# Optimization experiments

Measured on AMD Instinct MI355X. Metric: run time of the kernel, lower is better.

The kernel has to match this reference:

```python
import jax, jax.numpy as jnp
import numpy as np

N, M, KNN, KUP, POS_DIM = 15872, 35637, 5, 20, 32


def _pos_emb_table(n, d):
    # transformer-style sinusoidal table (matches PosEmb._define_pos_emb)
    pos = np.arange(n, dtype=np.float32)[:, None]
    i2 = np.arange(0, d, 2, dtype=np.float32)
    div = 10000.0 ** (i2 / d)
    pe = np.zeros((n, d), dtype=np.float32)
    pe[:, 0::2] = np.sin(pos / div)
    pe[:, 1::2] = np.cos(pos / div)
    return jnp.asarray(pe)


def _lrelu(x):
    return jnp.where(x > 0, x, 0.2 * x)


def _gather(x, idx):
    # x: [B,n,d], idx: [B,m,k] -> [B,m,k,d]
    return jax.vmap(lambda xb, ib: xb[ib])(x, idx)


def _knn_idx(x, k):
    # x: [B,n,d]; k nearest excluding self (torch knn drops column 0 of topk)
    xx = jnp.sum(x * x, axis=-1)
    neg = 2.0 * jnp.einsum('bnd,bmd->bnm', x, x) - xx[:, :, None] - xx[:, None, :]
    _, idx = jax.lax.top_k(neg, k + 1)
    return idx[..., 1:]


def _emb_block(feat, idx, ec_w1, ec_s1, ec_h1, ec_w2, ec_b2,
               w1, s1, h1, w2, s2, h2, w3, s3, h3, w4, b4):
    # get_graph_feature: [B,n,k,2*in] = cat(nbr - ctr, ctr)
    nbr = _gather(feat, idx)
    ctr = jnp.broadcast_to(feat[:, :, None, :], nbr.shape)
    e = jnp.concatenate([nbr - ctr, ctr], axis=-1)
    # edge_conv (1x1 conv2d = per-edge linear); BN folded into scale/shift (eval mode)
    e = _lrelu(jnp.einsum('bnkc,oc->bnko', e, ec_w1) * ec_s1 + ec_h1)
    e = jnp.einsum('bnkc,oc->bnko', e, ec_w2) + ec_b2
    f1 = jnp.max(e, axis=2)                                   # max over k neighbors -> [B,n,out]
    fmax = jnp.broadcast_to(jnp.max(f1, axis=1, keepdims=True), f1.shape)
    favg = jnp.broadcast_to(jnp.mean(f1, axis=1, keepdims=True), f1.shape)
    h = jnp.concatenate([feat, f1, fmax, favg], axis=-1)      # [B,n,3*out+in]
    # fc_out: 1x1 conv1d stack = per-point MLP with folded BN + LeakyReLU
    h = _lrelu(h @ w1.T * s1 + h1)
    h = _lrelu(h @ w2.T * s2 + h2)
    h = _lrelu(h @ w3.T * s3 + h3)
    return h @ w4.T + b4


def _forward(lx, ldx, pos_emb,
             b0_ec_w1, b0_ec_s1, b0_ec_h1, b0_ec_w2, b0_ec_b2,
             b0_fc_w1, b0_fc_s1, b0_fc_h1, b0_fc_w2, b0_fc_s2, b0_fc_h2,
             b0_fc_w3, b0_fc_s3, b0_fc_h3, b0_fc_w4, b0_fc_b4,
             b1_ec_w1, b1_ec_s1, b1_ec_h1, b1_ec_w2, b1_ec_b2,
             b1_fc_w1, b1_fc_s1, b1_fc_h1, b1_fc_w2, b1_fc_s2, b1_fc_h2,
             b1_fc_w3, b1_fc_s3, b1_fc_h3, b1_fc_w4, b1_fc_b4,
             up_inputs, up_w0, up_s0, up_h0, up_w_rest, up_s_rest, up_h_rest, up_wf, up_bf,
             dec_w0, dec_b0, dec_w1, dec_b1, dec_w2, dec_b2, dec_w3, dec_b3,
             dec_w4, dec_b4, dec_wf, dec_bf,
             idx0, up_idx):
    B = ldx.shape[0]
    feat_in = jnp.concatenate([ldx, jnp.broadcast_to(pos_emb[None], (B,) + pos_emb.shape)], axis=-1)  # [B,N,35]
    f0 = _emb_block(feat_in, idx0,
                    b0_ec_w1, b0_ec_s1, b0_ec_h1, b0_ec_w2, b0_ec_b2,
                    b0_fc_w1, b0_fc_s1, b0_fc_h1, b0_fc_w2, b0_fc_s2, b0_fc_h2,
                    b0_fc_w3, b0_fc_s3, b0_fc_h3, b0_fc_w4, b0_fc_b4)   # [B,N,64]
    idx1 = _knn_idx(f0, KNN)                                            # dynamic feature-space KNN
    f1 = _emb_block(f0, idx1,
                    b1_ec_w1, b1_ec_s1, b1_ec_h1, b1_ec_w2, b1_ec_b2,
                    b1_fc_w1, b1_fc_s1, b1_fc_h1, b1_fc_w2, b1_fc_s2, b1_fc_h2,
                    b1_fc_w3, b1_fc_s3, b1_fc_h3, b1_fc_w4, b1_fc_b4)   # [B,N,128]
    x_feat = jnp.concatenate([feat_in, f0, f1], axis=-1)                # [B,N,227]
    # Upscale: SIREN-activated 1x1-conv stack -> softmax interpolation weights over KUP lo-res nbrs
    h = jnp.sin(jnp.einsum('bmkc,oc->bmko', up_inputs[:B], up_w0) * up_s0 + up_h0)
    for i in range(up_w_rest.shape[0]):
        h = jnp.sin(jnp.einsum('bmkc,oc->bmko', h, up_w_rest[i]) * up_s_rest[i] + up_h_rest[i])
    logits = jnp.einsum('bmkc,oc->bmko', h, up_wf) + up_bf              # [B,M,KUP,1]
    w = jax.nn.softmax(logits, axis=2)
    grouped = _gather(x_feat, up_idx)                                   # [B,M,KUP,227]
    z = jnp.sum(w * grouped, axis=2)                                    # [B,M,227]
    # SIREN decoder: dims [227,256,128,64,32,16,3]; zip with 5 mods applies first 5 layers + head
    h = jnp.sin(30.0 * (z @ dec_w0.T + dec_b0))
    h = jnp.sin(h @ dec_w1.T + dec_b1)
    h = jnp.sin(h @ dec_w2.T + dec_b2)
    h = jnp.sin(h @ dec_w3.T + dec_b3)
    h = jnp.sin(h @ dec_w4.T + dec_b4)
    return h @ dec_wf.T + dec_bf                                        # [B,M,3]


def setup_inputs():
    key = jax.random.key(0)
    ks = iter(jax.random.split(key, 100))
    def rn(*s):
        return jax.random.normal(next(ks), s, jnp.float32) * 0.05
    def sc(*s):
        return jax.random.uniform(next(ks), s, jnp.float32, minval=0.5, maxval=1.5)
    inp = {}
    inp['lx'] = jax.random.normal(next(ks), (1, N, 3), jnp.float32)
    inp['ldx'] = jax.random.normal(next(ks), (1, N, 3), jnp.float32)
    inp['pos_emb'] = _pos_emb_table(N, POS_DIM)
    inp['idx0'] = jax.random.randint(next(ks), (1, N, KNN), 0, N - 1)
    # EmbModule 0: in=35, out=64
    inp['b0_ec_w1'], inp['b0_ec_s1'], inp['b0_ec_h1'] = rn(128, 70), sc(128), rn(128)
    inp['b0_ec_w2'], inp['b0_ec_b2'] = rn(64, 128), rn(64)
    inp['b0_fc_w1'], inp['b0_fc_s1'], inp['b0_fc_h1'] = rn(192, 227), sc(192), rn(192)
    inp['b0_fc_w2'], inp['b0_fc_s2'], inp['b0_fc_h2'] = rn(128, 192), sc(128), rn(128)
    inp['b0_fc_w3'], inp['b0_fc_s3'], inp['b0_fc_h3'] = rn(64, 128), sc(64), rn(64)
    inp['b0_fc_w4'], inp['b0_fc_b4'] = rn(64, 64), rn(64)
    # EmbModule 1: in=64, out=128
    inp['b1_ec_w1'], inp['b1_ec_s1'], inp['b1_ec_h1'] = rn(256, 128), sc(256), rn(256)
    inp['b1_ec_w2'], inp['b1_ec_b2'] = rn(128, 256), rn(128)
    inp['b1_fc_w1'], inp['b1_fc_s1'], inp['b1_fc_h1'] = rn(384, 448), sc(384), rn(384)
    inp['b1_fc_w2'], inp['b1_fc_s2'], inp['b1_fc_h2'] = rn(256, 384), sc(256), rn(256)
    inp['b1_fc_w3'], inp['b1_fc_s3'], inp['b1_fc_h3'] = rn(128, 256), sc(128), rn(128)
    inp['b1_fc_w4'], inp['b1_fc_b4'] = rn(128, 128), rn(128)
    inp['up_inputs'] = jax.random.uniform(next(ks), (1, M, KUP, 7), jnp.float32)
    inp['up_idx'] = jax.random.randint(next(ks), (1, M, KUP), 0, N - 1)
    inp['up_w0'], inp['up_s0'], inp['up_h0'] = rn(128, 7), sc(128), rn(128)
    inp['up_w_rest'], inp['up_s_rest'], inp['up_h_rest'] = rn(7, 128, 128), sc(7, 128), rn(7, 128)
    inp['up_wf'], inp['up_bf'] = rn(1, 128), rn(1)
    # SIREN decoder
    dd = [227, 256, 128, 64, 32, 16]
    for i in range(5):
        inp['dec_w%d' % i], inp['dec_b%d' % i] = rn(dd[i + 1], dd[i]), rn(dd[i + 1])
    inp['dec_wf'], inp['dec_bf'] = rn(3, 16), rn(3)
    return inp


def reference(lx, ldx, pos_emb, idx0,
              b0_ec_w1, b0_ec_s1, b0_ec_h1, b0_ec_w2, b0_ec_b2,
              b0_fc_w1, b0_fc_s1, b0_fc_h1, b0_fc_w2, b0_fc_s2, b0_fc_h2,
              b0_fc_w3, b0_fc_s3, b0_fc_h3, b0_fc_w4, b0_fc_b4,
              b1_ec_w1, b1_ec_s1, b1_ec_h1, b1_ec_w2, b1_ec_b2,
              b1_fc_w1, b1_fc_s1, b1_fc_h1, b1_fc_w2, b1_fc_s2, b1_fc_h2,
              b1_fc_w3, b1_fc_s3, b1_fc_h3, b1_fc_w4, b1_fc_b4,
              up_inputs, up_idx, up_w0, up_s0, up_h0,
              up_w_rest, up_s_rest, up_h_rest, up_wf, up_bf,
              dec_w0, dec_b0, dec_w1, dec_b1, dec_w2, dec_b2, dec_w3, dec_b3,
              dec_w4, dec_b4, dec_wf, dec_bf):
    return _forward(lx, ldx, pos_emb,
                    b0_ec_w1, b0_ec_s1, b0_ec_h1, b0_ec_w2, b0_ec_b2,
                    b0_fc_w1, b0_fc_s1, b0_fc_h1, b0_fc_w2, b0_fc_s2, b0_fc_h2,
                    b0_fc_w3, b0_fc_s3, b0_fc_h3, b0_fc_w4, b0_fc_b4,
                    b1_ec_w1, b1_ec_s1, b1_ec_h1, b1_ec_w2, b1_ec_b2,
                    b1_fc_w1, b1_fc_s1, b1_fc_h1, b1_fc_w2, b1_fc_s2, b1_fc_h2,
                    b1_fc_w3, b1_fc_s3, b1_fc_h3, b1_fc_w4, b1_fc_b4,
                    up_inputs, up_w0, up_s0, up_h0, up_w_rest, up_s_rest, up_h_rest, up_wf, up_bf,
                    dec_w0, dec_b0, dec_w1, dec_b1, dec_w2, dec_b2, dec_w3, dec_b3,
                    dec_w4, dec_b4, dec_wf, dec_bf,
                    idx0, up_idx)
```

## Files before the change

kernel.cpp:

```cpp
#include <hip/hip_runtime.h>
#include <hip/hip_bf16.h>
#include <math.h>

#define N_PTS 15872
#define M_PTS 35637
#define KNN_K 5
#define KUP   20
#define UP_ROWS (M_PTS * KUP)
#define NTILE (N_PTS/32)
#define N_EDGE (N_PTS*KNN_K)
#define CDIV(a,b) (((a)+(b)-1)/(b))
#define INV2PI 0.15915494309189535f

typedef __hip_bfloat16 bf16;
typedef unsigned int uint;
typedef unsigned short ushort_t;
__device__ __forceinline__ float b2f(bf16 x){ return __bfloat162float(x); }

__device__ __forceinline__ uint f2bf_bits(float x){
  uint u = __float_as_uint(x);
  return (u + 0x7FFFu + ((u>>16)&1u)) >> 16;
}

__device__ __forceinline__ ushort_t f2h_bits(float x){
  union { _Float16 h; ushort_t u; } c; c.h = (_Float16)x; return c.u;
}

__device__ __forceinline__ float sinrev(float x){
#if __has_builtin(__builtin_amdgcn_sinf)
  return __builtin_amdgcn_sinf(x);
#else
  return __sinf(x * 6.283185307179586f);
#endif
}

typedef __attribute__((ext_vector_type(8))) short bf16x8;
typedef __attribute__((ext_vector_type(8))) _Float16 f16x8;
typedef __attribute__((ext_vector_type(2))) __fp16 fp16x2_t;
typedef __attribute__((ext_vector_type(16))) float f32x16;
union FragAB { bf16x8 v; uint u[4]; };
union FragB  { bf16x8 v; uint4 q; };
union FragH  { f16x8 v; uint4 q; _Float16 h[8]; };
union Acc16  { f32x16 v; float f[16]; };
union H2U    { fp16x2_t h; uint u; };

__global__ void flag_k(const uint* __restrict__ pos_raw, int* __restrict__ flag){
  if (threadIdx.x == 0 && blockIdx.x == 0)
    flag[0] = (pos_raw[0] == 0x3F800000u) ? 1 : 0;
}

struct CvtTab { const void* src[52]; int start[52]; };
__global__ __launch_bounds__(256) void cvt_all_k(CvtTab tab, float* __restrict__ dst,
                                                 const int* __restrict__ flag, int total){
  int i = blockIdx.x*256 + threadIdx.x;
  if (i >= total) return;
  int s = 0;
#pragma unroll 1
  for (int k = 1; k < 52; k++) if (tab.start[k] <= i) s = k;
  int off = i - tab.start[s];
  float v = flag[0] ? b2f(((const bf16*)tab.src[s])[off]) : ((const float*)tab.src[s])[off];
  dst[i] = v;
}

__global__ void packfrag16_k(const float* __restrict__ w, const float* __restrict__ sr,
                             ushort_t* __restrict__ out, int n){
  int i = blockIdx.x*256 + threadIdx.x;
  if (i >= n) return;
  int j = i & 7;
  int lam = (i >> 3) & 63;
  int fg = i >> 9;
  int t = fg & 3, ks = (fg >> 2) & 1, Q = (fg >> 3) & 3, l = fg >> 5;
  int nn = t*32 + (lam & 31);
  int kk = Q*32 + ks*16 + ((j>>2)<<3) + ((lam>>5)<<2) + (j&3);
  float x = w[l*16384 + nn*128 + kk] * sr[l*128 + nn] * INV2PI;
  out[i] = f2h_bits(x);
}

struct PackTab { const float* src[18]; int N[18], K[18], ldk[18], Kpad[18], start[18]; };
__global__ __launch_bounds__(256) void packw_all_k(PackTab t, ushort_t* __restrict__ whi,
                                                   ushort_t* __restrict__ wlo, int total){
  int i = blockIdx.x*256 + threadIdx.x;
  if (i >= total) return;
  int s = 0;
#pragma unroll 1
  for (int q = 1; q < 18; q++) if (t.start[q] <= i) s = q;
  int ii = i - t.start[s];
  int j = ii & 7;
  int lane = (ii >> 3) & 63;
  int fr = ii >> 9;
  int nq = t.Kpad[s] >> 5;
  int ks = fr & 1;
  int q  = (fr >> 1) % nq;
  int nt = (fr >> 1) / nq;
  int n = nt*32 + (lane & 31);
  int k = q*32 + ks*16 + (lane >> 5)*8 + j;
  float x = (n < t.N[s] && k < t.K[s]) ? t.src[s][(size_t)n*t.ldk[s] + k] : 0.f;
  uint hb = f2bf_bits(x);
  uint lb = f2bf_bits(x - __uint_as_float(hb << 16));
  whi[i] = (ushort_t)hb;
  wlo[i] = (ushort_t)lb;
}

__global__ void packknn_k(const float* __restrict__ xf, const float* __restrict__ nr,
                          ushort_t* __restrict__ ahi, ushort_t* __restrict__ alo,
                          ushort_t* __restrict__ bhi, ushort_t* __restrict__ blo){
  int i = blockIdx.x*256 + threadIdx.x;
  if (i >= NTILE*5*64*8) return;
  int e = i & 7;
  int lane = (i >> 3) & 63;
  int rest = i >> 9;
  int kc = rest % 5, jt = rest / 5;
  int n = jt*32 + (lane & 31);
  int k = kc*16 + (lane >> 5)*8 + e;
  float f = (k < 64) ? xf[(size_t)n*227 + 35 + k] : 0.f;
  float av, bv;
  if (k < 64)      { av = 2.f*f;   bv = f; }
  else if (k == 64){ av = nr[n];   bv = -1.f; }
  else if (k == 65){ av = 1.f;     bv = -nr[n]; }
  else             { av = 0.f;     bv = 0.f; }
  uint ah = f2bf_bits(av); uint al = f2bf_bits(av - __uint_as_float(ah<<16));
  uint bh = f2bf_bits(bv); uint bl = f2bf_bits(bv - __uint_as_float(bh<<16));
  ahi[i] = (ushort_t)ah; alo[i] = (ushort_t)al;
  bhi[i] = (ushort_t)bh; blo[i] = (ushort_t)bl;
}

__global__ void fillmark_k(bf16* __restrict__ out, int n){
  int i = blockIdx.x*256 + threadIdx.x;
  if (i < n) out[i] = __float2bfloat16(12345.0f);
}

template<int ACT>
__global__ __launch_bounds__(256) void gemm_mfma_k(
    const float* __restrict__ A, int lda, int K, int M,
    const ushort_t* __restrict__ wh, const ushort_t* __restrict__ wl,
    int woff, int KqTot,
    const float* __restrict__ scale, const float* __restrict__ shift,
    float* __restrict__ C, int ldc, int N)
{
  __shared__ __align__(16) uint slab[64*128];
  const int tid = threadIdx.x;
  const int lane = tid & 63;
  const int wv = tid >> 6;
  const int np = lane & 31;
  const int hb2 = lane >> 5;
  const int rhalf = wv & 1, thalf = wv >> 1;
  const int rb = blockIdx.x * 64;
  const int tbase = blockIdx.y * 4;
  const int row_l = rhalf*32 + np;
  int NtLoc = (N >> 5) - tbase; if (NtLoc > 4) NtLoc = 4;

  Acc16 acc[2];
#pragma unroll
  for (int u=0;u<2;u++)
#pragma unroll
    for (int i=0;i<16;i++) acc[u].f[i] = 0.f;

#pragma unroll 1
  for (int k0 = 0; k0 < K; k0 += 128) {
    for (int e = tid; e < 64*32; e += 256) {
      int r = e >> 5, g = e & 31;
      int gr = rb + r;
      uint p[4];
#pragma unroll
      for (int u=0;u<4;u++){
        int k = k0 + g*4 + u;
        float f = (gr < M && k < K) ? A[(size_t)gr*lda + k] : 0.f;
        uint hb = f2bf_bits(f);
        uint lb = f2bf_bits(f - __uint_as_float(hb<<16));
        p[u] = (hb<<16) | lb;
      }
      *(uint4*)&slab[r*128 + (((g ^ r) & 31)<<2)] = make_uint4(p[0],p[1],p[2],p[3]);
    }
    __syncthreads();
    int qb = k0 >> 5;
    int KqLoc = KqTot - qb; if (KqLoc > 4) KqLoc = 4;
#pragma unroll 1
    for (int q = 0; q < KqLoc; q++){
#pragma unroll
      for (int ks = 0; ks < 2; ks++){
        int g0 = q*8 + ks*4 + hb2*2;
        uint4 a0 = *(const uint4*)&slab[row_l*128 + ((((g0  ) ^ row_l) & 31)<<2)];
        uint4 a1 = *(const uint4*)&slab[row_l*128 + ((((g0+1) ^ row_l) & 31)<<2)];
        uint au[8] = {a0.x,a0.y,a0.z,a0.w,a1.x,a1.y,a1.z,a1.w};
        FragAB ah, al;
#pragma unroll
        for (int p=0;p<4;p++){
          ah.u[p] = (au[2*p]>>16)     | (au[2*p+1] & 0xFFFF0000u);
          al.u[p] = (au[2*p]&0xFFFFu) | (au[2*p+1]<<16);
        }
#pragma unroll
        for (int u=0;u<2;u++){
          int t = thalf + u*2;
          if (t < NtLoc){
            size_t fb = (size_t)woff + ((size_t)(((tbase+t)*KqTot + qb + q)*2 + ks))*512 + (size_t)lane*8;
            FragB bh, bl;
            bh.q = *(const uint4*)(wh + fb);
            bl.q = *(const uint4*)(wl + fb);
            acc[u].v = __builtin_amdgcn_mfma_f32_32x32x16_bf16(ah.v, bh.v, acc[u].v, 0,0,0);
            acc[u].v = __builtin_amdgcn_mfma_f32_32x32x16_bf16(al.v, bh.v, acc[u].v, 0,0,0);
            acc[u].v = __builtin_amdgcn_mfma_f32_32x32x16_bf16(ah.v, bl.v, acc[u].v, 0,0,0);
          }
        }
      }
    }
    __syncthreads();
  }

#pragma unroll
  for (int u=0;u<2;u++){
    int t = thalf + u*2;
    if (t < NtLoc){
      int col = (tbase+t)*32 + np;
      float scv = scale[col], shv = shift[col];
#pragma unroll
      for (int reg=0;reg<16;reg++){
        int r32 = (reg&3) + 8*(reg>>2) + 4*hb2;
        int gr = rb + rhalf*32 + r32;
        if (gr < M){
          float v = acc[u].f[reg]*scv + shv;
          if (ACT==1) v = v > 0.f ? v : 0.2f*v;
          C[(size_t)gr*ldc + col] = v;
        }
      }
    }
  }
}

struct MLayer { int K, N, Kq, Nt, woff, soff, hoff, epi, act; float gmul; };
struct MCfg { MLayer L[6]; };

template<int NL, int OUTMODE>
__global__ __launch_bounds__(256) void mlp_fused_k(
    const float* __restrict__ A0, int lda0, int K0, int M,
    MCfg cfg,
    const ushort_t* __restrict__ wh, const ushort_t* __restrict__ wl,
    const float* __restrict__ wc,
    float* __restrict__ Cout, int ldc,
    void* __restrict__ oflg, const int* __restrict__ flag)
{
  __shared__ __align__(16) uint slab[64*256];
  const int tid = threadIdx.x;
  const int lane = tid & 63;
  const int wv = tid >> 6;
  const int np = lane & 31;
  const int hb2 = lane >> 5;
  const int rhalf = wv & 1, thalf = wv >> 1;
  const int rb = blockIdx.x * 64;
  const int row_l = rhalf*32 + np;

  for (int e = tid; e < 64*64; e += 256) {
    int r = e >> 6, g = e & 63;
    int gr = rb + r;
    uint p[4];
#pragma unroll
    for (int u=0;u<4;u++){
      int k = g*4+u;
      float f = (gr < M && k < K0) ? A0[(size_t)gr*lda0 + k] : 0.f;
      uint hb = f2bf_bits(f);
      uint lb = f2bf_bits(f - __uint_as_float(hb<<16));
      p[u] = (hb<<16) | lb;
    }
    *(uint4*)&slab[r*256 + (((g ^ r) & 63)<<2)] = make_uint4(p[0],p[1],p[2],p[3]);
  }
  __syncthreads();

#pragma unroll 1
  for (int l = 0; l < NL; l++){
    const int N = cfg.L[l].N, Kq = cfg.L[l].Kq, Nt = cfg.L[l].Nt;
    const int woff = cfg.L[l].woff, soff = cfg.L[l].soff, hoff = cfg.L[l].hoff;
    const int epi = cfg.L[l].epi, actf = cfg.L[l].act;
    const float gmul = cfg.L[l].gmul;
    Acc16 acc[4];
#pragma unroll
    for (int u=0;u<4;u++)
#pragma unroll
      for (int i=0;i<16;i++) acc[u].f[i] = 0.f;

#pragma unroll 1
    for (int q = 0; q < Kq; q++){
#pragma unroll
      for (int ks = 0; ks < 2; ks++){
        int g0 = (q*32 + ks*16 + hb2*8) >> 2;
        uint4 a0 = *(const uint4*)&slab[row_l*256 + ((((g0  ) ^ row_l) & 63)<<2)];
        uint4 a1 = *(const uint4*)&slab[row_l*256 + ((((g0+1) ^ row_l) & 63)<<2)];
        uint au[8] = {a0.x,a0.y,a0.z,a0.w,a1.x,a1.y,a1.z,a1.w};
        FragAB ah, al;
#pragma unroll
        for (int p=0;p<4;p++){
          ah.u[p] = (au[2*p]>>16)     | (au[2*p+1] & 0xFFFF0000u);
          al.u[p] = (au[2*p]&0xFFFFu) | (au[2*p+1]<<16);
        }
#pragma unroll
        for (int u=0;u<4;u++){
          int t = thalf + u*2;
          if (t < Nt){
            size_t fb = (size_t)woff + ((size_t)((t*Kq + q)*2 + ks))*512 + (size_t)lane*8;
            FragB bh, bl;
            bh.q = *(const uint4*)(wh + fb);
            bl.q = *(const uint4*)(wl + fb);
            acc[u].v = __builtin_amdgcn_mfma_f32_32x32x16_bf16(ah.v, bh.v, acc[u].v, 0,0,0);
            acc[u].v = __builtin_amdgcn_mfma_f32_32x32x16_bf16(al.v, bh.v, acc[u].v, 0,0,0);
            acc[u].v = __builtin_amdgcn_mfma_f32_32x32x16_bf16(ah.v, bl.v, acc[u].v, 0,0,0);
          }
        }
      }
    }
    __syncthreads();
#pragma unroll
    for (int u=0;u<4;u++){
      int t = thalf + u*2;
      if (t < Nt){
        int col = t*32 + np;
        if (col < N){
          float scv = (epi==0) ? wc[soff+col] : 0.f;
          float shv = wc[hoff+col];
#pragma unroll
          for (int reg=0;reg<16;reg++){
            int r32 = (reg&3) + 8*(reg>>2) + 4*hb2;
            float v = acc[u].f[reg];
            if (epi==0)      v = v*scv + shv;
            else if (epi==1) v = v + shv;
            else             v = (v + shv)*gmul;
            if (actf==1)      v = v > 0.f ? v : 0.2f*v;
            else if (actf==2) v = __sinf(v);
            if (l == NL-1){
              int gr = rb + rhalf*32 + r32;
              if (gr < M){
                if (OUTMODE==0) Cout[(size_t)gr*ldc + col] = v;
                else {
                  if (!(fabsf(v) < 1e30f)) v = 777.0f;
                  size_t oi = (size_t)gr*3 + col;
                  if (flag[0]) ((bf16*)oflg)[oi] = __float2bfloat16(v);
                  else         ((float*)oflg)[oi] = v;
                }
              }
            } else {
              int r = rhalf*32 + r32;
              uint hb = f2bf_bits(v);
              uint lb = f2bf_bits(v - __uint_as_float(hb<<16));
              slab[r*256 + ((((col>>2) ^ r) & 63)<<2) + (col&3)] = (hb<<16) | lb;
            }
          }
        }
      }
    }
    __syncthreads();
  }
}

#define INS5(tv, tj, v, j) \
  if ((v) > tv[4]){ tv[4]=(v); tj[4]=(j); \
    _Pragma("unroll") \
    for (int q=4;q>0;q--) \
      if (tv[q] > tv[q-1]){ float tf=tv[q-1]; tv[q-1]=tv[q]; tv[q]=tf; \
                            int ti=tj[q-1]; tj[q-1]=tj[q]; tj[q]=ti; } }

__global__ __launch_bounds__(256) void knn_mfma_k(
    const ushort_t* __restrict__ ahi, const ushort_t* __restrict__ alo,
    const ushort_t* __restrict__ bhi, const ushort_t* __restrict__ blo,
    int* __restrict__ out)
{
  __shared__ float mv[4][32][5];
  __shared__ int   mjj[4][32][5];
  const int tid = threadIdx.x;
  const int lane = tid & 63;
  const int wv = tid >> 6;
  const int np = lane & 31;
  const int hb2 = lane >> 5;
  const int it = blockIdx.x;
  const int ig = it*32 + np;

  FragB vh[5], vl[5];
  {
    size_t bb = (size_t)(it*5)*512 + (size_t)lane*8;
#pragma unroll
    for (int kc=0;kc<5;kc++){
      vh[kc].q = *(const uint4*)(bhi + bb + kc*512);
      vl[kc].q = *(const uint4*)(blo + bb + kc*512);
    }
  }

  float tv[5] = {-1e30f,-1e30f,-1e30f,-1e30f,-1e30f};
  int   tj[5] = {0,0,0,0,0};

  FragB uh[5], ul[5], nh[5], nl[5];
  {
    size_t ab = (size_t)(wv*5)*512 + (size_t)lane*8;
#pragma unroll
    for (int kc=0;kc<5;kc++){
      uh[kc].q = *(const uint4*)(ahi + ab + kc*512);
      ul[kc].q = *(const uint4*)(alo + ab + kc*512);
    }
  }

#pragma unroll 1
  for (int t = 0; t < NTILE/4; t++){
    int jt = wv + t*4;
    if (t+1 < NTILE/4){
      size_t an = (size_t)((jt+4)*5)*512 + (size_t)lane*8;
#pragma unroll
      for (int kc=0;kc<5;kc++){
        nh[kc].q = *(const uint4*)(ahi + an + kc*512);
        nl[kc].q = *(const uint4*)(alo + an + kc*512);
      }
    }
    Acc16 acc;
#pragma unroll
    for (int q=0;q<16;q++) acc.f[q] = 0.f;
#pragma unroll
    for (int kc=0;kc<5;kc++){
      acc.v = __builtin_amdgcn_mfma_f32_32x32x16_bf16(uh[kc].v, vh[kc].v, acc.v, 0,0,0);
      acc.v = __builtin_amdgcn_mfma_f32_32x32x16_bf16(ul[kc].v, vh[kc].v, acc.v, 0,0,0);
      acc.v = __builtin_amdgcn_mfma_f32_32x32x16_bf16(uh[kc].v, vl[kc].v, acc.v, 0,0,0);
    }
    int jb = jt*32 + 4*hb2;
#pragma unroll
    for (int reg=0;reg<16;reg++){
      int j = jb + (reg&3) + 8*(reg>>2);
      float v = acc.f[reg];
      if (j != ig) { INS5(tv, tj, v, j); }
    }
    if (t+1 < NTILE/4){
#pragma unroll
      for (int kc=0;kc<5;kc++){ uh[kc] = nh[kc]; ul[kc] = nl[kc]; }
    }
  }

#pragma unroll
  for (int s=0;s<5;s++){
    float ov = __shfl_xor(tv[s], 32, 64);
    int   oj = __shfl_xor(tj[s], 32, 64);
    INS5(tv, tj, ov, oj);
  }
  if (hb2 == 0){
#pragma unroll
    for (int s=0;s<5;s++){ mv[wv][np][s] = tv[s]; mjj[wv][np][s] = tj[s]; }
  }
  __syncthreads();
  if (tid < 32){
    float bv[5]; int bj[5];
#pragma unroll
    for (int s=0;s<5;s++){ bv[s] = mv[0][tid][s]; bj[s] = mjj[0][tid][s]; }
#pragma unroll
    for (int w=1;w<4;w++)
#pragma unroll
      for (int s=0;s<5;s++){
        float v = mv[w][tid][s]; int j = mjj[w][tid][s];
        INS5(bv, bj, v, j);
      }
    int gi = it*32 + tid;
#pragma unroll
    for (int s=0;s<5;s++) out[gi*KNN_K + s] = bj[s];
  }
}

__global__ __launch_bounds__(256) void siren_fused_k(
    const void* __restrict__ upin,
    const ushort_t* __restrict__ wf16,
    const float* __restrict__ W0c, const float* __restrict__ S0c, const float* __restrict__ H0c,
    const float* __restrict__ HRc,
    const float* __restrict__ WFc, const float* __restrict__ BFc,
    float* __restrict__ logits, const int* __restrict__ flag)
{
  __shared__ float intile[4*32*8];
  __shared__ __align__(16) float w0s[128*8];
  __shared__ __align__(16) float hrs[7*128];
  __shared__ __align__(16) float wfs[128];
  __shared__ float bfs[1];

  const int tid  = threadIdx.x;
  const int lane = tid & 63;
  const int wv   = tid >> 6;
  const int np   = lane & 31;
  const int hb2  = lane >> 5;
  const int rowbase = blockIdx.x * 128 + wv * 32;
  const int isbf = flag[0];
  float* intw = intile + wv*32*8;

  for (int e = tid; e < 128*7; e += 256){
    int c = e/7, k = e%7;
    w0s[c*8+k] = W0c[e]*S0c[c]*INV2PI;
  }
  if (tid < 128) w0s[tid*8+7] = H0c[tid]*INV2PI;
  for (int e = tid; e < 7*128; e += 256) hrs[e] = HRc[e]*INV2PI;
  if (tid < 128) wfs[tid] = WFc[tid];
  if (tid == 0) bfs[0] = BFc[0];
  for (int e = lane; e < 32*7; e += 64) {
    int r = e/7, k = e%7;
    int gr = rowbase + r;
    float v = 0.f;
    if (gr < UP_ROWS)
      v = isbf ? b2f(((const bf16*)upin)[(size_t)gr*7+k]) : ((const float*)upin)[(size_t)gr*7+k];
    intw[r*8+k] = v;
  }
  __syncthreads();

  uint st0[16], st1[16];
  {
    float xin[7];
#pragma unroll
    for (int k=0;k<7;k++) xin[k] = intw[np*8+k];
#pragma unroll
    for (int g = 0; g < 16; g++){
      float xs[4];
#pragma unroll
      for (int j = 0; j < 4; j++){
        int c = g*8 + hb2*4 + j;
        const float4 wa = *(const float4*)&w0s[c*8];
        const float4 wb = *(const float4*)&w0s[c*8+4];
        float a = wb.w;
        a += xin[0]*wa.x; a += xin[1]*wa.y; a += xin[2]*wa.z; a += xin[3]*wa.w;
        a += xin[4]*wb.x; a += xin[5]*wb.y; a += xin[6]*wb.z;
        xs[j] = sinrev(a);
      }
      H2U u0,u1;
      u0.h = __builtin_amdgcn_cvt_pkrtz(xs[0],xs[1]);
      u1.h = __builtin_amdgcn_cvt_pkrtz(xs[2],xs[3]);
      st0[g] = u0.u; st1[g] = u1.u;
    }
  }

  FragH fr[8];
#pragma unroll
  for (int m = 0; m < 8; m++)
    fr[m].q = make_uint4(st0[2*m], st1[2*m], st0[2*m+1], st1[2*m+1]);

  uint nst0[16], nst1[16];
#pragma unroll 1
  for (int l = 0; l < 7; l++) {
#pragma unroll
    for (int tp = 0; tp < 2; tp++){
      Acc16 acc0, acc1;
#pragma unroll
      for (int i=0;i<16;i++){ acc0.f[i] = 0.f; acc1.f[i] = 0.f; }
#pragma unroll
      for (int m = 0; m < 8; m++){
        int fb = (((l*8 + m)*4 + tp*2) << 9) + lane*8;
        FragH bh0, bh1;
        bh0.q = *(const uint4*)(wf16 + fb);
        bh1.q = *(const uint4*)(wf16 + fb + 512);
        acc0.v = __builtin_amdgcn_mfma_f32_32x32x16_f16(bh0.v, fr[m].v, acc0.v, 0,0,0);
        acc1.v = __builtin_amdgcn_mfma_f32_32x32x16_f16(bh1.v, fr[m].v, acc1.v, 0,0,0);
      }
#pragma unroll
      for (int rg = 0; rg < 4; rg++){
        int g0 = (tp*2+0)*4 + rg;
        const float4 b0v = *(const float4*)&hrs[l*128 + g0*8 + hb2*4];
        float x0 = sinrev(acc0.f[rg*4+0] + b0v.x);
        float x1 = sinrev(acc0.f[rg*4+1] + b0v.y);
        float x2 = sinrev(acc0.f[rg*4+2] + b0v.z);
        float x3 = sinrev(acc0.f[rg*4+3] + b0v.w);
        H2U u0,u1;
        u0.h = __builtin_amdgcn_cvt_pkrtz(x0,x1);
        u1.h = __builtin_amdgcn_cvt_pkrtz(x2,x3);
        nst0[g0] = u0.u; nst1[g0] = u1.u;

        int g1 = (tp*2+1)*4 + rg;
        const float4 b1v = *(const float4*)&hrs[l*128 + g1*8 + hb2*4];
        float y0 = sinrev(acc1.f[rg*4+0] + b1v.x);
        float y1 = sinrev(acc1.f[rg*4+1] + b1v.y);
        float y2 = sinrev(acc1.f[rg*4+2] + b1v.z);
        float y3 = sinrev(acc1.f[rg*4+3] + b1v.w);
        H2U v0,v1;
        v0.h = __builtin_amdgcn_cvt_pkrtz(y0,y1);
        v1.h = __builtin_amdgcn_cvt_pkrtz(y2,y3);
        nst0[g1] = v0.u; nst1[g1] = v1.u;
      }
    }
    if (l < 6){
#pragma unroll
      for (int m = 0; m < 8; m++)
        fr[m].q = make_uint4(nst0[2*m], nst1[2*m], nst0[2*m+1], nst1[2*m+1]);
    }
  }

  {
    float a = 0.f;
#pragma unroll
    for (int g = 0; g < 16; g++){
      const float4 w4 = *(const float4*)&wfs[g*8 + hb2*4];
      H2U u0,u1; u0.u = nst0[g]; u1.u = nst1[g];
      a += (float)u0.h.x*w4.x + (float)u0.h.y*w4.y
         + (float)u1.h.x*w4.z + (float)u1.h.y*w4.w;
    }
    a += __shfl_xor(a, 32, 64);
    int gr = rowbase + np;
    if (hb2 == 0 && gr < UP_ROWS) logits[gr] = a + bfs[0];
  }
}

__global__ void featin_k(const void* __restrict__ ldx, const void* __restrict__ pos,
                         float* __restrict__ xf, const int* __restrict__ flag){
  int i = blockIdx.x*256 + threadIdx.x;
  if (i >= N_PTS*35) return;
  int n = i / 35, c = i % 35;
  float v;
  if (flag[0]) {
    v = (c < 3) ? b2f(((const bf16*)ldx)[n*3+c]) : b2f(((const bf16*)pos)[n*32 + (c-3)]);
  } else {
    v = (c < 3) ? ((const float*)ldx)[n*3+c] : ((const float*)pos)[n*32 + (c-3)];
  }
  xf[(size_t)n*227 + c] = v;
}

__global__ void gather_e_k(const float* __restrict__ xf, int coff, int CIN,
                           const int* __restrict__ idx, float* __restrict__ e,
                           int n0, int np){
  int W2 = 2*CIN;
  int i = blockIdx.x*256 + threadIdx.x;
  if (i >= np*KNN_K*W2) return;
  int c = i % W2; int ek = i / W2;
  int nl = ek / KNN_K, k = ek % KNN_K;
  int n = n0 + nl;
  int j = idx[n*KNN_K + k];
  float out;
  if (c < CIN) out = xf[(size_t)j*227 + coff + c] - xf[(size_t)n*227 + coff + c];
  else         out = xf[(size_t)n*227 + coff + (c-CIN)];
  e[(size_t)ek*W2 + c] = out;
}

__global__ void kmax_k(const float* __restrict__ e2, int C, int ld, float* __restrict__ f1,
                       int n0, int np){
  int i = blockIdx.x*256 + threadIdx.x;
  if (i >= np*C) return;
  int nl = i / C, c = i % C;
  float v = -1e30f;
  for (int k=0;k<KNN_K;k++) v = fmaxf(v, e2[((size_t)nl*KNN_K+k)*ld + c]);
  f1[(size_t)(n0+nl)*C + c] = v;
}

template<int C>
__global__ __launch_bounds__(256) void reduce1_k(const float* __restrict__ X, int n,
                                                 float* __restrict__ pmax, float* __restrict__ psum){
  const int tid = threadIdx.x;
  const int c = tid % C;
  const int r0 = tid / C;
  const int TPR = 256 / C;
  float vmax = -1e30f, vsum = 0.f;
  for (int row = blockIdx.x * TPR + r0; row < n; row += gridDim.x * TPR) {
    float v = X[(size_t)row * C + c];
    vmax = fmaxf(vmax, v); vsum += v;
  }
  __shared__ float smax[256], ssum[256];
  smax[tid]=vmax; ssum[tid]=vsum;
  __syncthreads();
  if (tid < C) {
    for (int q=1;q<TPR;q++){ vmax=fmaxf(vmax, smax[q*C+c]); vsum += ssum[q*C+c]; }
    pmax[blockIdx.x*C + c] = vmax; psum[blockIdx.x*C + c] = vsum;
  }
}

template<int C>
__global__ __launch_bounds__(256) void red2fold_k(
    const float* __restrict__ pmax, const float* __restrict__ psum,
    int nblk, float invn,
    const float* __restrict__ W, int ldw, int off1, int off2,
    const float* __restrict__ scale, const float* __restrict__ shift,
    float* __restrict__ out, int N)
{
  __shared__ float smax[C], ssum[C];
  int tid = threadIdx.x;
  if (tid < C){
    float vmax=-1e30f, vsum=0.f;
    for (int b=0;b<nblk;b++){ vmax=fmaxf(vmax,pmax[b*C+tid]); vsum+=psum[b*C+tid]; }
    smax[tid]=vmax; ssum[tid]=vsum*invn;
  }
  __syncthreads();
  for (int n = tid; n < N; n += 256){
    const float* wr = W + (size_t)n*ldw;
    float s = 0.f;
    for (int j=0;j<C;j++) s += wr[off1+j]*smax[j];
    for (int j=0;j<C;j++) s += wr[off2+j]*ssum[j];
    out[n] = s*scale[n] + shift[n];
  }
}

__global__ void concat2_k(const float* __restrict__ xf, int coff, int CF,
                          const float* __restrict__ f1, int C,
                          float* __restrict__ h, int n0, int np){
  int W = CF + C;
  int i = blockIdx.x*256 + threadIdx.x;
  if (i >= np*W) return;
  int nl = i / W, c = i % W;
  int n = n0 + nl;
  float v = (c < CF) ? xf[(size_t)n*227 + coff + c] : f1[(size_t)n*C + (c-CF)];
  h[(size_t)nl*W + c] = v;
}

__global__ void norms_k(const float* __restrict__ xf, float* __restrict__ nr){
  int n = blockIdx.x*256 + threadIdx.x;
  if (n >= N_PTS) return;
  const float* p = xf + (size_t)n*227 + 35;
  float s = 0.f;
  for (int d=0;d<64;d++) s += p[d]*p[d];
  nr[n] = s;
}

__global__ __launch_bounds__(256) void softgather_k(const float* __restrict__ logits,
                                                    const int* __restrict__ up_idx,
                                                    const float* __restrict__ xf,
                                                    float* __restrict__ z){
  __shared__ float lw[4][KUP]; __shared__ int li[4][KUP];
  int sub = threadIdx.x >> 6;
  int tid = threadIdx.x & 63;
  int m = blockIdx.x*4 + sub;
  bool ok = (m < M_PTS);
  if (ok && tid < KUP){
    lw[sub][tid] = logits[(size_t)m*KUP + tid];
    li[sub][tid] = up_idx[(size_t)m*KUP + tid];
  }
  __syncthreads();
  if (ok){
    float mx = -1e30f;
    for (int k=0;k<KUP;k++) mx = fmaxf(mx, lw[sub][k]);
    float w[KUP]; float s = 0.f;
    for (int k=0;k<KUP;k++){ w[k] = expf(lw[sub][k]-mx); s += w[k]; }
    float inv = 1.f/s;
    for (int c = tid; c < 227; c += 64){
      float acc = 0.f;
      for (int k=0;k<KUP;k++) acc += w[k] * xf[(size_t)li[sub][k]*227 + c];
      z[(size_t)m*227 + c] = acc*inv;
    }
  }
}

extern "C" void kernel_launch(void* const* d_in, const int* in_sizes, int n_in,
                              void* d_out, int out_size, void* d_ws, size_t ws_size,
                              hipStream_t stream) {
  const int *idx0  = (const int*)d_in[3];
  const int *upidx = (const int*)d_in[37];

  float* ws = (float*)d_ws;
  float* x_feat = ws;
  float* f1b    = ws + 3602944;
  float* pmax   = ws + 5634560;
  float* psum   = ws + 5667328;
  float* fold0  = pmax + 24576;
  float* fold1  = psum + 24576;
  int*   flag   = (int*)(ws + 5700352);
  int*   idx1   = (int*)(ws + 5700368);
  float* nrm    = ws + 5779728;
  float* logits = ws + 5795600;
  float* wcvt   = ws + 6508352;
  float* S      = ws + 7214400;
  ushort_t* whi  = (ushort_t*)(S + 9662464);
  ushort_t* wlo  = whi + 114688;
  ushort_t* gwhi = wlo + 114688;
  ushort_t* gwlo = gwhi + 503808;

  const size_t NEED = (size_t)(7214400 + 9662464) * 4
                    + (size_t)(114688*2 + 503808*2) * 2;
  if (ws_size < NEED) {
    fillmark_k<<<CDIV(out_size,256),256,0,stream>>>((bf16*)d_out, out_size);
    return;
  }

  flag_k<<<1,64,0,stream>>>((const uint*)d_in[2], flag);
  CvtTab tab;
  int wcoff = 0, seg = 0;
  auto CVT = [&](int i, int n)->const float* {
    tab.src[seg] = d_in[i]; tab.start[seg] = wcoff; seg++;
    const float* p = wcvt + wcoff; wcoff += n;
    return p;
  };
  const float *E0W1=CVT(4,8960),  *E0S1=CVT(5,128),  *E0H1=CVT(6,128),
              *E0W2=CVT(7,8192),  *E0B2=CVT(8,64);
  const float *F0W1=CVT(9,43584), *F0S1=CVT(10,192), *F0H1=CVT(11,192),
              *F0W2=CVT(12,24576),*F0S2=CVT(13,128), *F0H2=CVT(14,128),
              *F0W3=CVT(15,8192), *F0S3=CVT(16,64),  *F0H3=CVT(17,64),
              *F0W4=CVT(18,4096), *F0B4=CVT(19,64);
  const float *E1W1=CVT(20,32768),*E1S1=CVT(21,256), *E1H1=CVT(22,256),
              *E1W2=CVT(23,32768),*E1B2=CVT(24,128);
  const float *F1W1=CVT(25,172032),*F1S1=CVT(26,384),*F1H1=CVT(27,384),
              *F1W2=CVT(28,98304),*F1S2=CVT(29,256), *F1H2=CVT(30,256),
              *F1W3=CVT(31,32768),*F1S3=CVT(32,128), *F1H3=CVT(33,128),
              *F1W4=CVT(34,16384),*F1B4=CVT(35,128);
  const float *UPW0=CVT(38,896),  *UPS0=CVT(39,128), *UPH0=CVT(40,128),
              *UPWR=CVT(41,114688),*UPSR=CVT(42,896),*UPHR=CVT(43,896),
              *UPWF=CVT(44,128),  *UPBF=CVT(45,1);
  const float *DW0=CVT(46,58112), *DB0=CVT(47,256),
              *DW1=CVT(48,32768), *DB1=CVT(49,128),
              *DW2=CVT(50,8192),  *DB2=CVT(51,64),
              *DW3=CVT(52,2048),  *DB3=CVT(53,32),
              *DW4=CVT(54,512),   *DB4=CVT(55,16),
              *DWF=CVT(56,48),    *DBF=CVT(57,3);
  cvt_all_k<<<CDIV(wcoff,256),256,0,stream>>>(tab, wcvt, flag, wcoff);

  packfrag16_k<<<CDIV(114688,256),256,0,stream>>>(UPWR, UPSR, whi, 114688);

  PackTab ptab;
  int offs[18];
  int ptotal = 0;
  {
    int q = 0;
    auto REG = [&](const float* s, int N, int K, int ldk, int Kpad){
      ptab.src[q]=s; ptab.N[q]=N; ptab.K[q]=K; ptab.ldk[q]=ldk; ptab.Kpad[q]=Kpad;
      ptab.start[q]=ptotal; offs[q]=ptotal;
      ptotal += CDIV(N,32)*32*Kpad; q++;
    };
    REG(F0W1,192, 99,227,128);
    REG(F0W2,128,192,192,192); REG(F0W3,64,128,128,128); REG(F0W4,64,64,64,64);
    REG(DW0,256,227,227,256);  REG(DW1,128,256,256,256);  REG(DW2,64,128,128,128);
    REG(DW3,32,64,64,64);      REG(DW4,16,32,32,32);      REG(DWF,3,16,16,32);
    REG(E0W1,128,70,70,96);    REG(E0W2,64,128,128,128);
    REG(E1W1,256,128,128,128); REG(E1W2,128,256,256,256);
    REG(F1W3,128,256,256,256); REG(F1W4,128,128,128,128);
    REG(F1W1,384,192,448,192);
    REG(F1W2,256,384,384,384);
  }
  packw_all_k<<<CDIV(ptotal,256),256,0,stream>>>(ptab, gwhi, gwlo, ptotal);

  auto OFF = [&](const float* p){ return (int)(p - wcvt); };
  const int HOFF0 = (int)(fold0 - wcvt);
  MCfg cfc0{};
  cfc0.L[0] = { 99,192,4,6, offs[0], OFF(F0S1), HOFF0,     0,1, 0.f};
  cfc0.L[1] = {192,128,6,4, offs[1], OFF(F0S2), OFF(F0H2), 0,1, 0.f};
  cfc0.L[2] = {128, 64,4,2, offs[2], OFF(F0S3), OFF(F0H3), 0,1, 0.f};
  cfc0.L[3] = { 64, 64,2,2, offs[3], 0,         OFF(F0B4), 1,0, 0.f};
  MCfg cdec{};
  cdec.L[0] = {227,256,8,8, offs[4], 0, OFF(DB0), 2,2, 30.f};
  cdec.L[1] = {256,128,8,4, offs[5], 0, OFF(DB1), 1,2, 0.f};
  cdec.L[2] = {128, 64,4,2, offs[6], 0, OFF(DB2), 1,2, 0.f};
  cdec.L[3] = { 64, 32,2,1, offs[7], 0, OFF(DB3), 1,2, 0.f};
  cdec.L[4] = { 32, 16,1,1, offs[8], 0, OFF(DB4), 1,2, 0.f};
  cdec.L[5] = { 16,  3,1,1, offs[9], 0, OFF(DBF), 1,0, 0.f};
  MCfg ce0{};
  ce0.L[0] = { 70,128,3,4, offs[10], OFF(E0S1), OFF(E0H1), 0,1, 0.f};
  ce0.L[1] = {128, 64,4,2, offs[11], 0,         OFF(E0B2), 1,0, 0.f};
  MCfg ce1{};
  ce1.L[0] = {128,256,4,8, offs[12], OFF(E1S1), OFF(E1H1), 0,1, 0.f};
  ce1.L[1] = {256,128,8,4, offs[13], 0,         OFF(E1B2), 1,0, 0.f};
  MCfg cf1t{};
  cf1t.L[0] = {256,128,8,4, offs[14], OFF(F1S3), OFF(F1H3), 0,1, 0.f};
  cf1t.L[1] = {128,128,4,4, offs[15], 0,         OFF(F1B4), 1,0, 0.f};

  const float invN = 1.f/(float)N_PTS;

  featin_k<<<CDIV(N_PTS*35,256),256,0,stream>>>(d_in[1], d_in[2], x_feat, flag);

  {
    float* eA = S;
    gather_e_k<<<CDIV(N_EDGE*70,256),256,0,stream>>>(x_feat, 0, 35, idx0, eA, 0, N_PTS);
    mlp_fused_k<2,0><<<CDIV(N_EDGE,64),256,0,stream>>>(
        eA,70,70,N_EDGE, ce0, gwhi,gwlo,wcvt, eA,70, nullptr, flag);
    kmax_k<<<CDIV(N_PTS*64,256),256,0,stream>>>(eA, 64, 70, f1b, 0, N_PTS);
  }
  reduce1_k<64><<<256,256,0,stream>>>(f1b, N_PTS, pmax, psum);
  red2fold_k<64><<<1,256,0,stream>>>(pmax, psum, 256, invN,
                                     F0W1,227, 99,163, F0S1,F0H1, fold0, 192);
  {
    float* h = S;
    concat2_k<<<CDIV(N_PTS*99,256),256,0,stream>>>(x_feat,0,35, f1b,64, h, 0, N_PTS);
    mlp_fused_k<4,0><<<CDIV(N_PTS,64),256,0,stream>>>(
        h,99,99,N_PTS, cfc0, gwhi,gwlo,wcvt, x_feat+35,227, nullptr, flag);
  }

  norms_k<<<CDIV(N_PTS,256),256,0,stream>>>(x_feat, nrm);
  {
    const int PLANE = NTILE*5*64*8;
    ushort_t* ajhi = (ushort_t*)S;
    ushort_t* ajlo = ajhi + PLANE;
    ushort_t* bihi = ajlo + PLANE;
    ushort_t* bilo = bihi + PLANE;
    packknn_k<<<CDIV(PLANE,256),256,0,stream>>>(x_feat, nrm, ajhi, ajlo, bihi, bilo);
    knn_mfma_k<<<NTILE,256,0,stream>>>(ajhi, ajlo, bihi, bilo, idx1);
  }

  {
    const int P1 = 7936;
    for (int n0 = 0; n0 < N_PTS; n0 += P1) {
      int np = N_PTS - n0; if (np > P1) np = P1;
      int ne = np * KNN_K;
      float* eA = S;
      gather_e_k<<<CDIV(ne*128,256),256,0,stream>>>(x_feat, 35, 64, idx1, eA, n0, np);
      mlp_fused_k<2,0><<<CDIV(ne,64),256,0,stream>>>(
          eA,128,128,ne, ce1, gwhi,gwlo,wcvt, eA,128, nullptr, flag);
      kmax_k<<<CDIV(np*128,256),256,0,stream>>>(eA, 128, 128, f1b, n0, np);
    }
  }
  reduce1_k<128><<<256,256,0,stream>>>(f1b, N_PTS, pmax, psum);
  red2fold_k<128><<<1,256,0,stream>>>(pmax, psum, 256, invN,
                                      F1W1,448, 192,320, F1S1,F1H1, fold1, 384);
  {
    float* h  = S;
    float* a1 = S + 3047424;
    int gx = CDIV(N_PTS,64);
    concat2_k<<<CDIV(N_PTS*192,256),256,0,stream>>>(x_feat,35,64, f1b,128, h, 0, N_PTS);
    gemm_mfma_k<1><<<dim3(gx,3),256,0,stream>>>(h,192,192,N_PTS, gwhi,gwlo, offs[16],6,
                                                F1S1,fold1, a1,384, 384);
    gemm_mfma_k<1><<<dim3(gx,2),256,0,stream>>>(a1,384,384,N_PTS, gwhi,gwlo, offs[17],12,
                                                F1S2,F1H2, h,256, 256);
    mlp_fused_k<2,0><<<gx,256,0,stream>>>(
        h,256,256,N_PTS, cf1t, gwhi,gwlo,wcvt, x_feat+99,227, nullptr, flag);
  }

  siren_fused_k<<<CDIV(UP_ROWS,128),256,0,stream>>>(
      d_in[36], whi, UPW0, UPS0, UPH0, UPHR, UPWF, UPBF, logits, flag);
  float* zbuf = S;
  softgather_k<<<CDIV(M_PTS,4),256,0,stream>>>(logits, upidx, x_feat, zbuf);

  mlp_fused_k<6,1><<<CDIV(M_PTS,64),256,0,stream>>>(
      zbuf,227,227,M_PTS, cdec, gwhi,gwlo,wcvt, nullptr,0, d_out, flag);
}
```

Measured before the change: 1.759 ms.

## Fuse edge gather into edge MLP and softmax-gather into decoder MLP

Adds two kernels. One builds edge features (neighbour minus centre, plus centre) straight into shared memory inside the edge-conv MLP. The other computes the softmax-weighted upsampling gather directly into the decoder MLP's shared-memory slab. This drops the separate gather and softgather kernels and their global-memory round trips through intermediate buffers. The trade-off is that scattered gather loads now happen inside the MFMA kernel's prologue, where occupancy is limited by the large shared slab, so latency may be less well hidden.

Result: slower. 1.999 ms (+13.6%).

```diff
diff --git a/kernel.cpp b/kernel.cpp
--- a/kernel.cpp
+++ b/kernel.cpp
@@ -348,6 +348,272 @@
   }
 }
 
+template<int NL>
+__global__ __launch_bounds__(256) void mlp_edge_k(
+    const float* __restrict__ xf, int coff, int CIN,
+    const int* __restrict__ idx, int n0, int M ,
+    MCfg cfg,
+    const ushort_t* __restrict__ wh, const ushort_t* __restrict__ wl,
+    const float* __restrict__ wc,
+    float* __restrict__ Cout, int ldc)
+{
+  __shared__ __align__(16) uint slab[64*256];
+  const int tid = threadIdx.x;
+  const int lane = tid & 63;
+  const int wv = tid >> 6;
+  const int np = lane & 31;
+  const int hb2 = lane >> 5;
+  const int rhalf = wv & 1, thalf = wv >> 1;
+  const int rb = blockIdx.x * 64;
+  const int row_l = rhalf*32 + np;
+  const int W2 = 2*CIN;
+
+  for (int e = tid; e < 64*64; e += 256) {
+    int r = e >> 6, g = e & 63;
+    int ek = rb + r;
+    int n = 0, j = 0;
+    bool ok = (ek < M);
+    if (ok){
+      n = n0 + ek/KNN_K;
+      j = idx[n*KNN_K + ek%KNN_K];
+    }
+    uint p[4];
+#pragma unroll
+    for (int u=0;u<4;u++){
+      int k = g*4+u;
+      float f = 0.f;
+      if (ok && k < W2){
+        f = (k < CIN) ? xf[(size_t)j*227 + coff + k] - xf[(size_t)n*227 + coff + k]
+                      : xf[(size_t)n*227 + coff + (k-CIN)];
+      }
+      uint hb = f2bf_bits(f);
+      uint lb = f2bf_bits(f - __uint_as_float(hb<<16));
+      p[u] = (hb<<16) | lb;
+    }
+    *(uint4*)&slab[r*256 + (((g ^ r) & 63)<<2)] = make_uint4(p[0],p[1],p[2],p[3]);
+  }
+  __syncthreads();
+
+#pragma unroll 1
+  for (int l = 0; l < NL; l++){
+    const int N = cfg.L[l].N, Kq = cfg.L[l].Kq, Nt = cfg.L[l].Nt;
+    const int woff = cfg.L[l].woff, soff = cfg.L[l].soff, hoff = cfg.L[l].hoff;
+    const int epi = cfg.L[l].epi, actf = cfg.L[l].act;
+    Acc16 acc[4];
+#pragma unroll
+    for (int u=0;u<4;u++)
+#pragma unroll
+      for (int i=0;i<16;i++) acc[u].f[i] = 0.f;
+
+#pragma unroll 1
+    for (int q = 0; q < Kq; q++){
+#pragma unroll
+      for (int ks = 0; ks < 2; ks++){
+        int g0 = (q*32 + ks*16 + hb2*8) >> 2;
+        uint4 a0 = *(const uint4*)&slab[row_l*256 + ((((g0  ) ^ row_l) & 63)<<2)];
+        uint4 a1 = *(const uint4*)&slab[row_l*256 + ((((g0+1) ^ row_l) & 63)<<2)];
+        uint au[8] = {a0.x,a0.y,a0.z,a0.w,a1.x,a1.y,a1.z,a1.w};
+        FragAB ah, al;
+#pragma unroll
+        for (int p=0;p<4;p++){
+          ah.u[p] = (au[2*p]>>16)     | (au[2*p+1] & 0xFFFF0000u);
+          al.u[p] = (au[2*p]&0xFFFFu) | (au[2*p+1]<<16);
+        }
+#pragma unroll
+        for (int u=0;u<4;u++){
+          int t = thalf + u*2;
+          if (t < Nt){
+            size_t fb = (size_t)woff + ((size_t)((t*Kq + q)*2 + ks))*512 + (size_t)lane*8;
+            FragB bh, bl;
+            bh.q = *(const uint4*)(wh + fb);
+            bl.q = *(const uint4*)(wl + fb);
+            acc[u].v = __builtin_amdgcn_mfma_f32_32x32x16_bf16(ah.v, bh.v, acc[u].v, 0,0,0);
+            acc[u].v = __builtin_amdgcn_mfma_f32_32x32x16_bf16(al.v, bh.v, acc[u].v, 0,0,0);
+            acc[u].v = __builtin_amdgcn_mfma_f32_32x32x16_bf16(ah.v, bl.v, acc[u].v, 0,0,0);
+          }
+        }
+      }
+    }
+    __syncthreads();
+#pragma unroll
+    for (int u=0;u<4;u++){
+      int t = thalf + u*2;
+      if (t < Nt){
+        int col = t*32 + np;
+        if (col < N){
+          float scv = (epi==0) ? wc[soff+col] : 0.f;
+          float shv = wc[hoff+col];
+#pragma unroll
+          for (int reg=0;reg<16;reg++){
+            int r32 = (reg&3) + 8*(reg>>2) + 4*hb2;
+            float v = acc[u].f[reg];
+            if (epi==0)      v = v*scv + shv;
+            else             v = v + shv;
+            if (actf==1)     v = v > 0.f ? v : 0.2f*v;
+            if (l == NL-1){
+              int gr = rb + rhalf*32 + r32;
+              if (gr < M) Cout[(size_t)gr*ldc + col] = v;
+            } else {
+              int r = rhalf*32 + r32;
+              uint hb = f2bf_bits(v);
+              uint lb = f2bf_bits(v - __uint_as_float(hb<<16));
+              slab[r*256 + ((((col>>2) ^ r) & 63)<<2) + (col&3)] = (hb<<16) | lb;
+            }
+          }
+        }
+      }
+    }
+    __syncthreads();
+  }
+}
+
+__global__ __launch_bounds__(256) void mlp_dec_k(
+    const float* __restrict__ logits, const int* __restrict__ up_idx,
+    const float* __restrict__ xf, int M,
+    MCfg cfg,
+    const ushort_t* __restrict__ wh, const ushort_t* __restrict__ wl,
+    const float* __restrict__ wc,
+    void* __restrict__ oflg, const int* __restrict__ flag)
+{
+  __shared__ __align__(16) uint slab[64*256];
+  __shared__ float lwd[64][KUP];
+  __shared__ int   lid[64][KUP];
+  const int tid = threadIdx.x;
+  const int lane = tid & 63;
+  const int wv = tid >> 6;
+  const int np = lane & 31;
+  const int hb2 = lane >> 5;
+  const int rhalf = wv & 1, thalf = wv >> 1;
+  const int rb = blockIdx.x * 64;
+  const int row_l = rhalf*32 + np;
+
+  for (int p = tid; p < 64*KUP; p += 256){
+    int r = p / KUP, k = p % KUP;
+    int gr = rb + r;
+    if (gr < M){
+      lwd[r][k] = logits[(size_t)gr*KUP + k];
+      lid[r][k] = up_idx[(size_t)gr*KUP + k];
+    } else { lwd[r][k] = 0.f; lid[r][k] = 0; }
+  }
+  __syncthreads();
+  if (tid < 64){
+    int gr = rb + tid;
+    if (gr < M){
+      float mx = -1e30f;
+#pragma unroll 1
+      for (int k=0;k<KUP;k++) mx = fmaxf(mx, lwd[tid][k]);
+      float s = 0.f;
+#pragma unroll 1
+      for (int k=0;k<KUP;k++){ float w = expf(lwd[tid][k]-mx); lwd[tid][k] = w; s += w; }
+      float inv = 1.f/s;
+#pragma unroll 1
+      for (int k=0;k<KUP;k++) lwd[tid][k] *= inv;
+    } else {
+#pragma unroll 1
+      for (int k=0;k<KUP;k++) lwd[tid][k] = 0.f;
+    }
+  }
+  __syncthreads();
+  for (int e = tid; e < 64*64; e += 256){
+    int r = e >> 6, g = e & 63;
+    int cb = g*4;
+    float f0=0.f, f1=0.f, f2=0.f, f3=0.f;
+#pragma unroll 1
+    for (int k=0;k<KUP;k++){
+      float w = lwd[r][k];
+      const float* src = xf + (size_t)lid[r][k]*227 + cb;
+      f0 += w*src[0]; f1 += w*src[1]; f2 += w*src[2]; f3 += w*src[3];
+    }
+    float fv[4] = {f0,f1,f2,f3};
+    uint p[4];
+#pragma unroll
+    for (int u=0;u<4;u++){
+      uint hb = f2bf_bits(fv[u]);
+      uint lb = f2bf_bits(fv[u] - __uint_as_float(hb<<16));
+      p[u] = (hb<<16) | lb;
+    }
+    *(uint4*)&slab[r*256 + (((g ^ r) & 63)<<2)] = make_uint4(p[0],p[1],p[2],p[3]);
+  }
+  __syncthreads();
+
+#pragma unroll 1
+  for (int l = 0; l < 6; l++){
+    const int N = cfg.L[l].N, Kq = cfg.L[l].Kq, Nt = cfg.L[l].Nt;
+    const int woff = cfg.L[l].woff, hoff = cfg.L[l].hoff;
+    const int epi = cfg.L[l].epi, actf = cfg.L[l].act;
+    const float gmul = cfg.L[l].gmul;
+    Acc16 acc[4];
+#pragma unroll
+    for (int u=0;u<4;u++)
+#pragma unroll
+      for (int i=0;i<16;i++) acc[u].f[i] = 0.f;
+
+#pragma unroll 1
+    for (int q = 0; q < Kq; q++){
+#pragma unroll
+      for (int ks = 0; ks < 2; ks++){
+        int g0 = (q*32 + ks*16 + hb2*8) >> 2;
+        uint4 a0 = *(const uint4*)&slab[row_l*256 + ((((g0  ) ^ row_l) & 63)<<2)];
+        uint4 a1 = *(const uint4*)&slab[row_l*256 + ((((g0+1) ^ row_l) & 63)<<2)];
+        uint au[8] = {a0.x,a0.y,a0.z,a0.w,a1.x,a1.y,a1.z,a1.w};
+        FragAB ah, al;
+#pragma unroll
+        for (int p=0;p<4;p++){
+          ah.u[p] = (au[2*p]>>16)     | (au[2*p+1] & 0xFFFF0000u);
+          al.u[p] = (au[2*p]&0xFFFFu) | (au[2*p+1]<<16);
+        }
+#pragma unroll
+        for (int u=0;u<4;u++){
+          int t = thalf + u*2;
+          if (t < Nt){
+            size_t fb = (size_t)woff + ((size_t)((t*Kq + q)*2 + ks))*512 + (size_t)lane*8;
+            FragB bh, bl;
+            bh.q = *(const uint4*)(wh + fb);
+            bl.q = *(const uint4*)(wl + fb);
+            acc[u].v = __builtin_amdgcn_mfma_f32_32x32x16_bf16(ah.v, bh.v, acc[u].v, 0,0,0);
+            acc[u].v = __builtin_amdgcn_mfma_f32_32x32x16_bf16(al.v, bh.v, acc[u].v, 0,0,0);
+            acc[u].v = __builtin_amdgcn_mfma_f32_32x32x16_bf16(ah.v, bl.v, acc[u].v, 0,0,0);
+          }
+        }
+      }
+    }
+    __syncthreads();
+#pragma unroll
+    for (int u=0;u<4;u++){
+      int t = thalf + u*2;
+      if (t < Nt){
+        int col = t*32 + np;
+        if (col < N){
+          float shv = wc[hoff+col];
+#pragma unroll
+          for (int reg=0;reg<16;reg++){
+            int r32 = (reg&3) + 8*(reg>>2) + 4*hb2;
+            float v = acc[u].f[reg];
+            if (epi==1) v = v + shv;
+            else        v = (v + shv)*gmul;
+            if (actf==2) v = __sinf(v);
+            if (l == 5){
+              int gr = rb + rhalf*32 + r32;
+              if (gr < M){
+                if (!(fabsf(v) < 1e30f)) v = 777.0f;
+                size_t oi = (size_t)gr*3 + col;
+                if (flag[0]) ((bf16*)oflg)[oi] = __float2bfloat16(v);
+                else         ((float*)oflg)[oi] = v;
+              }
+            } else {
+              int r = rhalf*32 + r32;
+              uint hb = f2bf_bits(v);
+              uint lb = f2bf_bits(v - __uint_as_float(hb<<16));
+              slab[r*256 + ((((col>>2) ^ r) & 63)<<2) + (col&3)] = (hb<<16) | lb;
+            }
+          }
+        }
+      }
+    }
+    __syncthreads();
+  }
+}
+
 #define INS5(tv, tj, v, j) \
   if ((v) > tv[4]){ tv[4]=(v); tj[4]=(j); \
     _Pragma("unroll") \
@@ -603,22 +869,6 @@
   xf[(size_t)n*227 + c] = v;
 }
 
-__global__ void gather_e_k(const float* __restrict__ xf, int coff, int CIN,
-                           const int* __restrict__ idx, float* __restrict__ e,
-                           int n0, int np){
-  int W2 = 2*CIN;
-  int i = blockIdx.x*256 + threadIdx.x;
-  if (i >= np*KNN_K*W2) return;
-  int c = i % W2; int ek = i / W2;
-  int nl = ek / KNN_K, k = ek % KNN_K;
-  int n = n0 + nl;
-  int j = idx[n*KNN_K + k];
-  float out;
-  if (c < CIN) out = xf[(size_t)j*227 + coff + c] - xf[(size_t)n*227 + coff + c];
-  else         out = xf[(size_t)n*227 + coff + (c-CIN)];
-  e[(size_t)ek*W2 + c] = out;
-}
-
 __global__ void kmax_k(const float* __restrict__ e2, int C, int ld, float* __restrict__ f1,
                        int n0, int np){
   int i = blockIdx.x*256 + threadIdx.x;
@@ -694,34 +944,6 @@
   float s = 0.f;
   for (int d=0;d<64;d++) s += p[d]*p[d];
   nr[n] = s;
-}
-
-__global__ __launch_bounds__(256) void softgather_k(const float* __restrict__ logits,
-                                                    const int* __restrict__ up_idx,
-                                                    const float* __restrict__ xf,
-                                                    float* __restrict__ z){
-  __shared__ float lw[4][KUP]; __shared__ int li[4][KUP];
-  int sub = threadIdx.x >> 6;
-  int tid = threadIdx.x & 63;
-  int m = blockIdx.x*4 + sub;
-  bool ok = (m < M_PTS);
-  if (ok && tid < KUP){
-    lw[sub][tid] = logits[(size_t)m*KUP + tid];
-    li[sub][tid] = up_idx[(size_t)m*KUP + tid];
-  }
-  __syncthreads();
-  if (ok){
-    float mx = -1e30f;
-    for (int k=0;k<KUP;k++) mx = fmaxf(mx, lw[sub][k]);
-    float w[KUP]; float s = 0.f;
-    for (int k=0;k<KUP;k++){ w[k] = expf(lw[sub][k]-mx); s += w[k]; }
-    float inv = 1.f/s;
-    for (int c = tid; c < 227; c += 64){
-      float acc = 0.f;
-      for (int k=0;k<KUP;k++) acc += w[k] * xf[(size_t)li[sub][k]*227 + c];
-      z[(size_t)m*227 + c] = acc*inv;
-    }
-  }
 }
 
 extern "C" void kernel_launch(void* const* d_in, const int* in_sizes, int n_in,
@@ -839,11 +1061,10 @@
   featin_k<<<CDIV(N_PTS*35,256),256,0,stream>>>(d_in[1], d_in[2], x_feat, flag);
 
   {
-    float* eA = S;
-    gather_e_k<<<CDIV(N_EDGE*70,256),256,0,stream>>>(x_feat, 0, 35, idx0, eA, 0, N_PTS);
-    mlp_fused_k<2,0><<<CDIV(N_EDGE,64),256,0,stream>>>(
-        eA,70,70,N_EDGE, ce0, gwhi,gwlo,wcvt, eA,70, nullptr, flag);
-    kmax_k<<<CDIV(N_PTS*64,256),256,0,stream>>>(eA, 64, 70, f1b, 0, N_PTS);
+    float* eOut = S;
+    mlp_edge_k<2><<<CDIV(N_EDGE,64),256,0,stream>>>(
+        x_feat, 0, 35, idx0, 0, N_EDGE, ce0, gwhi,gwlo,wcvt, eOut,64);
+    kmax_k<<<CDIV(N_PTS*64,256),256,0,stream>>>(eOut, 64, 64, f1b, 0, N_PTS);
   }
   reduce1_k<64><<<256,256,0,stream>>>(f1b, N_PTS, pmax, psum);
   red2fold_k<64><<<1,256,0,stream>>>(pmax, psum, 256, invN,
@@ -871,11 +1092,10 @@
     for (int n0 = 0; n0 < N_PTS; n0 += P1) {
       int np = N_PTS - n0; if (np > P1) np = P1;
       int ne = np * KNN_K;
-      float* eA = S;
-      gather_e_k<<<CDIV(ne*128,256),256,0,stream>>>(x_feat, 35, 64, idx1, eA, n0, np);
-      mlp_fused_k<2,0><<<CDIV(ne,64),256,0,stream>>>(
-          eA,128,128,ne, ce1, gwhi,gwlo,wcvt, eA,128, nullptr, flag);
-      kmax_k<<<CDIV(np*128,256),256,0,stream>>>(eA, 128, 128, f1b, n0, np);
+      float* eOut = S;
+      mlp_edge_k<2><<<CDIV(ne,64),256,0,stream>>>(
+          x_feat, 35, 64, idx1, n0, ne, ce1, gwhi,gwlo,wcvt, eOut,128);
+      kmax_k<<<CDIV(np*128,256),256,0,stream>>>(eOut, 128, 128, f1b, n0, np);
     }
   }
   reduce1_k<128><<<256,256,0,stream>>>(f1b, N_PTS, pmax, psum);
@@ -896,9 +1116,7 @@
 
   siren_fused_k<<<CDIV(UP_ROWS,128),256,0,stream>>>(
       d_in[36], whi, UPW0, UPS0, UPH0, UPHR, UPWF, UPBF, logits, flag);
-  float* zbuf = S;
-  softgather_k<<<CDIV(M_PTS,4),256,0,stream>>>(logits, upidx, x_feat, zbuf);
-
-  mlp_fused_k<6,1><<<CDIV(M_PTS,64),256,0,stream>>>(
-      zbuf,227,227,M_PTS, cdec, gwhi,gwlo,wcvt, nullptr,0, d_out, flag);
-}
+
+  mlp_dec_k<<<CDIV(M_PTS,64),256,0,stream>>>(
+      logits, upidx, x_feat, M_PTS, cdec, gwhi,gwlo,wcvt, d_out, flag);
+}
```
